# Kernel tuning notes

Measured on AMD Instinct MI355X. Metric: run time of the kernel, lower is better.

Reference implementation:

```python
import jax, jax.numpy as jnp
import numpy as np

B, S, H = 32, 1024, 512
NEG = -1e10

def setup_inputs() -> dict:
    key = jax.random.key(0)
    k1, k2, k3, k4, k5, k6 = jax.random.split(key, 6)
    return {
        "hidden": jax.random.normal(k1, (B, H), jnp.float32),
        "encoder_outputs": jax.random.normal(k2, (B, S, 2 * H), jnp.float32),
        "mask": jax.random.randint(k3, (B, S), 0, 2, jnp.int32),
        "W_attn": jax.random.normal(k4, (3 * H, H), jnp.float32) * (1.0 / np.sqrt(3 * H)),
        "b_attn": jax.random.normal(k5, (H,), jnp.float32) * 0.01,
        "W_v": jax.random.normal(k6, (H,), jnp.float32) * (1.0 / np.sqrt(H)),
    }

def reference(hidden, encoder_outputs, mask, W_attn, b_attn, W_v):
    # Split the concat-matmul: cat([h, enc]) @ W_attn == h @ W_h + enc @ W_e
    W_h, W_e = W_attn[:H], W_attn[H:]            # [H,H], [2H,H]
    proj_h = hidden @ W_h                        # [B, H]
    proj_e = jnp.einsum('bse,eh->bsh', encoder_outputs, W_e)  # [B, S, H]
    energy = jnp.tanh(proj_h[:, None, :] + proj_e + b_attn)   # [B, S, H]
    scores = jnp.einsum('bsh,h->bs', energy, W_v)             # [B, S]
    scores = jnp.where(mask == 0, NEG, scores)
    attn_w = jax.nn.softmax(scores, axis=1)                   # [B, S]
    context = jnp.einsum('bs,bse->be', attn_w, encoder_outputs)  # [B, 2H]
    return context, attn_w
```

## Files before the change

### kernel.cpp

```cpp
#include <hip/hip_runtime.h>
#include <hip/hip_bf16.h>
#include <math.h>

#define NB 32
#define NS 1024
#define NH 512
#define NE 1024
#define NEGV -1e10f

typedef _Float16 f16x8 __attribute__((ext_vector_type(8)));
typedef _Float16 f16x4 __attribute__((ext_vector_type(4)));
typedef float f32x4 __attribute__((ext_vector_type(4)));

__device__ __forceinline__ float fast_tanh(float x) {
  float t = __expf(2.f * x);
  return (t - 1.f) * __builtin_amdgcn_rcpf(t + 1.f);
}

__global__ __launch_bounds__(256) void proj_h_kernel(
    const float* __restrict__ hidden, const float* __restrict__ W_attn,
    const float* __restrict__ b_attn, float* __restrict__ c) {
  int b = blockIdx.x >> 1;
  int h = ((blockIdx.x & 1) << 8) + threadIdx.x;
  __shared__ float hid[NH];
  for (int e = threadIdx.x; e < NH; e += 256) hid[e] = hidden[b * NH + e];
  __syncthreads();
  float acc = b_attn[h];
#pragma unroll 8
  for (int e = 0; e < NH; ++e) acc = fmaf(hid[e], W_attn[(size_t)e * NH + h], acc);
  c[b * NH + h] = acc;
}

__global__ __launch_bounds__(256) void prep_We_kernel(
    const float* __restrict__ W_attn, _Float16* __restrict__ Bp) {
  int ks = blockIdx.x;
  int t = threadIdx.x;
#pragma unroll
  for (int p = 0; p < 8; ++p) {
    int f = (p << 8) + t;
    int ws = f >> 8;
    int nj = (f >> 6) & 3;
    int lane = f & 63;
    int col = (ws << 6) + (nj << 4) + (lane & 15);
    int kb = (ks << 5) + ((lane >> 4) << 3);
    f16x8 h;
#pragma unroll
    for (int j = 0; j < 8; ++j)
      h[j] = (_Float16)W_attn[(size_t)(NH + kb + j) * NH + col];
    *(f16x8*)((char*)Bp + (size_t)(((ks << 3) + ws) << 12) + (nj << 10) + (lane << 4)) = h;
  }
}

__global__ __launch_bounds__(512) void score_kernel(
    const float* __restrict__ enc, const _Float16* __restrict__ Bp,
    const float* __restrict__ c, const float* __restrict__ Wv,
    float* __restrict__ spart) {
  __shared__ float Asm[2][64 * 64];
  const int tid = threadIdx.x;
  const int lane = tid & 63;
  const int wid = tid >> 6;
  const int r15 = lane & 15;
  const int id = blockIdx.x;
  const int mt = ((id & 7) << 6) + (id >> 3);
  const int b = mt >> 4;
  const int s0 = (mt & 15) << 6;
  const char* Abase = (const char*)(enc + ((size_t)b * NS + s0) * NE);
  const char* Bbase = (const char*)Bp + ((size_t)wid << 12);

  f32x4 acc[4][4];
#pragma unroll
  for (int i = 0; i < 4; ++i)
#pragma unroll
    for (int j = 0; j < 4; ++j) acc[i][j] = (f32x4)0.f;

#define STAGE_A(KT, BUF)                                                         \
  _Pragma("unroll") for (int i = 0; i < 2; ++i) {                                \
    int d = (i << 13) + (tid << 4);                                              \
    int row = d >> 8;                                                            \
    int sb = (d & 255) ^ ((row & 15) << 4);                                      \
    __builtin_amdgcn_global_load_lds(                                            \
        (const __attribute__((address_space(1))) uint32_t*)(Abase + (size_t)row * 4096 + ((size_t)(KT) << 8) + sb), \
        (__attribute__((address_space(3))) uint32_t*)((char*)Asm[BUF] + (i << 13) + (wid << 10)), \
        16, 0, 0);                                                               \
  }

#define BLOAD(ARR, KS)                                                           \
  _Pragma("unroll") for (int nj = 0; nj < 4; ++nj)                               \
      ARR[nj] = *(const f16x8*)(Bbase + ((size_t)(KS) << 15) +                   \
                                (nj << 10) + (lane << 4));

#define COMPUTE_KK(CUR, KK, ARR)                                                 \
  _Pragma("unroll") for (int mi = 0; mi < 4; ++mi) {                             \
    int row = (mi << 4) + r15;                                                   \
    int off1 = (row << 8) + ((KK) << 7) + ((lane >> 4) << 5);                    \
    int x = (row & 15) << 4;                                                     \
    f32x4 u = *(const f32x4*)((const char*)Asm[CUR] + (off1 ^ x));               \
    f32x4 v = *(const f32x4*)((const char*)Asm[CUR] + ((off1 + 16) ^ x));        \
    f16x8 h;                                                                     \
    h[0] = (_Float16)u[0]; h[1] = (_Float16)u[1];                                \
    h[2] = (_Float16)u[2]; h[3] = (_Float16)u[3];                                \
    h[4] = (_Float16)v[0]; h[5] = (_Float16)v[1];                                \
    h[6] = (_Float16)v[2]; h[7] = (_Float16)v[3];                                \
    _Pragma("unroll") for (int nj = 0; nj < 4; ++nj)                             \
      acc[mi][nj] = __builtin_amdgcn_mfma_f32_16x16x32_f16(h, ARR[nj],           \
                                                           acc[mi][nj], 0, 0, 0); \
  }

  f16x8 bfE[4], bfO[4];
  STAGE_A(0, 0);
  BLOAD(bfE, 0);
  __syncthreads();
  for (int kt = 0; kt < 16; kt += 2) {
    STAGE_A(kt + 1, 1);
    BLOAD(bfO, (kt << 1) + 1);
    COMPUTE_KK(0, 0, bfE);
    BLOAD(bfE, (kt << 1) + 2);
    COMPUTE_KK(0, 1, bfO);
    __syncthreads();
    if (kt < 14) STAGE_A(kt + 2, 0);
    BLOAD(bfO, (kt << 1) + 3);
    COMPUTE_KK(1, 0, bfE);
    if (kt < 14) BLOAD(bfE, (kt << 1) + 4);
    COMPUTE_KK(1, 1, bfO);
    __syncthreads();
  }
#undef STAGE_A
#undef BLOAD
#undef COMPUTE_KK

  float sr[4][4];
#pragma unroll
  for (int i = 0; i < 4; ++i)
#pragma unroll
    for (int r = 0; r < 4; ++r) sr[i][r] = 0.f;
#pragma unroll
  for (int nj = 0; nj < 4; ++nj) {
    int hcol = (wid << 6) + (nj << 4) + r15;
    float wvj = Wv[hcol];
    float cvj = c[b * NH + hcol];
#pragma unroll
    for (int mi = 0; mi < 4; ++mi)
#pragma unroll
      for (int r = 0; r < 4; ++r)
        sr[mi][r] += wvj * fast_tanh(acc[mi][nj][r] + cvj);
  }
#pragma unroll
  for (int off = 1; off < 16; off <<= 1)
#pragma unroll
    for (int mi = 0; mi < 4; ++mi)
#pragma unroll
      for (int r = 0; r < 4; ++r) sr[mi][r] += __shfl_xor(sr[mi][r], off, 64);
  if (r15 == 0) {
    float* dst = spart + (size_t)wid * NB * NS + b * NS + s0;
#pragma unroll
    for (int mi = 0; mi < 4; ++mi)
#pragma unroll
      for (int r = 0; r < 4; ++r)
        dst[(mi << 4) + ((lane >> 4) << 2) + r] = sr[mi][r];
  }
}

__global__ __launch_bounds__(256) void softmax_kernel(
    const float* __restrict__ spart, const int* __restrict__ mask,
    float* __restrict__ attn) {
  int b = blockIdx.x, tid = threadIdx.x;
  __shared__ float red[8];
  float v[4];
  float mx = -INFINITY;
#pragma unroll
  for (int j = 0; j < 4; ++j) {
    int s = tid + (j << 8);
    float x = 0.f;
#pragma unroll
    for (int p = 0; p < 8; ++p) x += spart[(size_t)p * NB * NS + b * NS + s];
    v[j] = (mask[b * NS + s] == 0) ? NEGV : x;
    mx = fmaxf(mx, v[j]);
  }
#pragma unroll
  for (int off = 32; off >= 1; off >>= 1) mx = fmaxf(mx, __shfl_xor(mx, off, 64));
  if ((tid & 63) == 0) red[tid >> 6] = mx;
  __syncthreads();
  mx = fmaxf(fmaxf(red[0], red[1]), fmaxf(red[2], red[3]));
  float sum = 0.f;
#pragma unroll
  for (int j = 0; j < 4; ++j) {
    v[j] = __expf(v[j] - mx);
    sum += v[j];
  }
#pragma unroll
  for (int off = 32; off >= 1; off >>= 1) sum += __shfl_xor(sum, off, 64);
  __syncthreads();
  if ((tid & 63) == 0) red[4 + (tid >> 6)] = sum;
  __syncthreads();
  float inv = 1.f / (red[4] + red[5] + red[6] + red[7]);
#pragma unroll
  for (int j = 0; j < 4; ++j) attn[b * NS + tid + (j << 8)] = v[j] * inv;
}

__global__ __launch_bounds__(256) void ctx_partial_kernel(
    const float* __restrict__ enc, const float* __restrict__ attn,
    float* __restrict__ partial) {
  int ch = blockIdx.x;
  int b = blockIdx.y;
  int tid = threadIdx.x;
  __shared__ float w[64];
  if (tid < 64) w[tid] = attn[b * NS + (ch << 6) + tid];
  __syncthreads();
  const float* encb = enc + ((size_t)b * NS + (ch << 6)) * NE;
  float4 acc = make_float4(0.f, 0.f, 0.f, 0.f);
  int e = tid << 2;
  for (int s = 0; s < 64; ++s) {
    float4 x = *(const float4*)(encb + (size_t)s * NE + e);
    float ws_ = w[s];
    acc.x = fmaf(ws_, x.x, acc.x);
    acc.y = fmaf(ws_, x.y, acc.y);
    acc.z = fmaf(ws_, x.z, acc.z);
    acc.w = fmaf(ws_, x.w, acc.w);
  }
  *(float4*)(partial + ((size_t)(b * 16 + ch)) * NE + e) = acc;
}

__global__ __launch_bounds__(256) void ctx_reduce_kernel(
    const float* __restrict__ partial, float* __restrict__ ctx) {
  int b = blockIdx.x;
  int e = threadIdx.x << 2;
  float4 acc = make_float4(0.f, 0.f, 0.f, 0.f);
  for (int ch = 0; ch < 16; ++ch) {
    float4 x = *(const float4*)(partial + ((size_t)(b * 16 + ch)) * NE + e);
    acc.x += x.x;
    acc.y += x.y;
    acc.z += x.z;
    acc.w += x.w;
  }
  *(float4*)(ctx + (size_t)b * NE + e) = acc;
}

extern "C" void kernel_launch(void* const* d_in, const int* in_sizes, int n_in,
                              void* d_out, int out_size, void* d_ws, size_t ws_size,
                              hipStream_t stream) {
  const float* hidden = (const float*)d_in[0];
  const float* enc = (const float*)d_in[1];
  const int* mask = (const int*)d_in[2];
  const float* W_attn = (const float*)d_in[3];
  const float* b_attn = (const float*)d_in[4];
  const float* W_v = (const float*)d_in[5];

  float* ctx = (float*)d_out;
  float* attn = ctx + NB * NS;

  char* ws = (char*)d_ws;
  float* c = (float*)ws;
  float* spart = (float*)(ws + 65536);
  float* partial = (float*)(ws + 65536 + 1048576);
  _Float16* Bp = (_Float16*)(ws + 65536 + 1048576 + 2097152);

  proj_h_kernel<<<64, 256, 0, stream>>>(hidden, W_attn, b_attn, c);
  prep_We_kernel<<<32, 256, 0, stream>>>(W_attn, Bp);
  score_kernel<<<512, 512, 0, stream>>>(enc, Bp, c, W_v, spart);
  softmax_kernel<<<NB, 256, 0, stream>>>(spart, mask, attn);
  ctx_partial_kernel<<<dim3(16, NB), 256, 0, stream>>>(enc, attn, partial);
  ctx_reduce_kernel<<<NB, 256, 0, stream>>>(partial, ctx);
}
```

Before: 115.3 us.

## Preload whole encoder tile as fp16 into LDS before MFMA loop

The score kernel stops double-buffering fp32 encoder slices through async global-to-LDS loads. It now loads the whole 64x1024 tile up front, converts it to fp16 once, and stores it in a 128KB swizzled LDS buffer. The MFMA loop then reads fp16 fragments directly, with no conversions and no barriers inside the loop. The trade-offs are that the load is no longer overlapped with compute, and the large LDS footprint limits occupancy to one block per CU.

```diff
diff --git a/kernel.cpp b/kernel.cpp
--- a/kernel.cpp
+++ b/kernel.cpp
@@ -55,7 +55,7 @@
     const float* __restrict__ enc, const _Float16* __restrict__ Bp,
     const float* __restrict__ c, const float* __restrict__ Wv,
     float* __restrict__ spart) {
-  __shared__ float Asm[2][64 * 64];
+  __shared__ _Float16 Afp16[64 * 1024];
   const int tid = threadIdx.x;
   const int lane = tid & 63;
   const int wid = tid >> 6;
@@ -64,69 +64,60 @@
   const int mt = ((id & 7) << 6) + (id >> 3);
   const int b = mt >> 4;
   const int s0 = (mt & 15) << 6;
-  const char* Abase = (const char*)(enc + ((size_t)b * NS + s0) * NE);
+  const float* encb = enc + ((size_t)b * NS + s0) * NE;
   const char* Bbase = (const char*)Bp + ((size_t)wid << 12);
 
+#pragma unroll 4
+  for (int p = 0; p < 32; ++p) {
+    int f = (p << 9) + tid;
+    int row = f >> 8;
+    int kq = f & 255;
+    float4 v = *(const float4*)(encb + ((size_t)row << 10) + (kq << 2));
+    f16x4 h;
+    h[0] = (_Float16)v.x; h[1] = (_Float16)v.y;
+    h[2] = (_Float16)v.z; h[3] = (_Float16)v.w;
+    int off = (row << 11) + (kq << 3);
+    off ^= (row & 7) << 4;
+    *(f16x4*)((char*)Afp16 + off) = h;
+  }
+  __syncthreads();
+
   f32x4 acc[4][4];
 #pragma unroll
   for (int i = 0; i < 4; ++i)
 #pragma unroll
     for (int j = 0; j < 4; ++j) acc[i][j] = (f32x4)0.f;
-
-#define STAGE_A(KT, BUF)                                                         \
-  _Pragma("unroll") for (int i = 0; i < 2; ++i) {                                \
-    int d = (i << 13) + (tid << 4);                                              \
-    int row = d >> 8;                                                            \
-    int sb = (d & 255) ^ ((row & 15) << 4);                                      \
-    __builtin_amdgcn_global_load_lds(                                            \
-        (const __attribute__((address_space(1))) uint32_t*)(Abase + (size_t)row * 4096 + ((size_t)(KT) << 8) + sb), \
-        (__attribute__((address_space(3))) uint32_t*)((char*)Asm[BUF] + (i << 13) + (wid << 10)), \
-        16, 0, 0);                                                               \
-  }
 
 #define BLOAD(ARR, KS)                                                           \
   _Pragma("unroll") for (int nj = 0; nj < 4; ++nj)                               \
       ARR[nj] = *(const f16x8*)(Bbase + ((size_t)(KS) << 15) +                   \
                                 (nj << 10) + (lane << 4));
 
-#define COMPUTE_KK(CUR, KK, ARR)                                                 \
-  _Pragma("unroll") for (int mi = 0; mi < 4; ++mi) {                             \
-    int row = (mi << 4) + r15;                                                   \
-    int off1 = (row << 8) + ((KK) << 7) + ((lane >> 4) << 5);                    \
-    int x = (row & 15) << 4;                                                     \
-    f32x4 u = *(const f32x4*)((const char*)Asm[CUR] + (off1 ^ x));               \
-    f32x4 v = *(const f32x4*)((const char*)Asm[CUR] + ((off1 + 16) ^ x));        \
-    f16x8 h;                                                                     \
-    h[0] = (_Float16)u[0]; h[1] = (_Float16)u[1];                                \
-    h[2] = (_Float16)u[2]; h[3] = (_Float16)u[3];                                \
-    h[4] = (_Float16)v[0]; h[5] = (_Float16)v[1];                                \
-    h[6] = (_Float16)v[2]; h[7] = (_Float16)v[3];                                \
-    _Pragma("unroll") for (int nj = 0; nj < 4; ++nj)                             \
-      acc[mi][nj] = __builtin_amdgcn_mfma_f32_16x16x32_f16(h, ARR[nj],           \
-                                                           acc[mi][nj], 0, 0, 0); \
+#define COMPUTE(KS, ARR)                                                         \
+  {                                                                              \
+    f16x8 af[4];                                                                 \
+    _Pragma("unroll") for (int mi = 0; mi < 4; ++mi) {                           \
+      int row = (mi << 4) + r15;                                                 \
+      int off = (row << 11) + ((KS) << 6) + ((lane >> 4) << 4);                  \
+      off ^= (row & 7) << 4;                                                     \
+      af[mi] = *(const f16x8*)((const char*)Afp16 + off);                        \
+    }                                                                            \
+    _Pragma("unroll") for (int mi = 0; mi < 4; ++mi)                             \
+      _Pragma("unroll") for (int nj = 0; nj < 4; ++nj)                           \
+        acc[mi][nj] = __builtin_amdgcn_mfma_f32_16x16x32_f16(af[mi], ARR[nj],    \
+                                                             acc[mi][nj], 0, 0, 0); \
   }
 
   f16x8 bfE[4], bfO[4];
-  STAGE_A(0, 0);
   BLOAD(bfE, 0);
-  __syncthreads();
-  for (int kt = 0; kt < 16; kt += 2) {
-    STAGE_A(kt + 1, 1);
-    BLOAD(bfO, (kt << 1) + 1);
-    COMPUTE_KK(0, 0, bfE);
-    BLOAD(bfE, (kt << 1) + 2);
-    COMPUTE_KK(0, 1, bfO);
-    __syncthreads();
-    if (kt < 14) STAGE_A(kt + 2, 0);
-    BLOAD(bfO, (kt << 1) + 3);
-    COMPUTE_KK(1, 0, bfE);
-    if (kt < 14) BLOAD(bfE, (kt << 1) + 4);
-    COMPUTE_KK(1, 1, bfO);
-    __syncthreads();
-  }
-#undef STAGE_A
+  for (int ks = 0; ks < 32; ks += 2) {
+    BLOAD(bfO, ks + 1);
+    COMPUTE(ks, bfE);
+    if (ks < 30) BLOAD(bfE, ks + 2);
+    COMPUTE(ks + 1, bfO);
+  }
 #undef BLOAD
-#undef COMPUTE_KK
+#undef COMPUTE
 
   float sr[4][4];
 #pragma unroll
```

Measured after the change: 106.7 us. 7.4% less time.
